# Kernel optimization log

Hardware: AMD Instinct MI355X
Metric: run time of the kernel (lower is better)

Reference implementation:

```python
import jax, jax.numpy as jnp
import numpy as np

# tiny-cuda-nn canonical 2D image hash-grid config
L = 16            # n_levels
F = 2             # n_features_per_level
T = 1 << 19       # hashmap size per level
BASE = 16         # base_resolution
SCALE = 1.5       # per_level_scale
HIDDEN = 64
ENC_DIM = L * F   # 32
OUT = 3           # rgb
S = 1024          # img_res / output_size
PRIME_Y = np.uint32(2654435761)


def setup_inputs() -> dict:
    key = jax.random.key(0)
    k1, k2, k3, k4 = jax.random.split(key, 4)
    # pixel-center grid exactly as in the torch module
    half = 0.5 / S
    xs = jnp.linspace(half, 1.0 - half, S, dtype=jnp.float32)
    xv, yv = jnp.meshgrid(xs, xs, indexing='ij')
    xy = jnp.stack([yv.flatten(), xv.flatten()], axis=1)  # [S*S, 2]
    # tcnn initializes hash tables ~ U(-1e-4, 1e-4)
    hash_tables = jax.random.uniform(k1, (L, T, F), jnp.float32, -1e-4, 1e-4)
    W0 = jax.random.normal(k2, (ENC_DIM, HIDDEN), jnp.float32) * np.sqrt(2.0 / ENC_DIM)
    W1 = jax.random.normal(k3, (HIDDEN, HIDDEN), jnp.float32) * np.sqrt(2.0 / HIDDEN)
    W2 = jax.random.normal(k4, (HIDDEN, OUT), jnp.float32) * np.sqrt(2.0 / HIDDEN)
    return {"xy": xy, "hash_tables": hash_tables, "W0": W0, "W1": W1, "W2": W2}


def _encode(xy, hash_tables):
    # multiresolution hash-grid encoding with bilinear interpolation
    resolutions = jnp.floor(BASE * SCALE ** jnp.arange(L)).astype(jnp.int32)  # [L]
    offs = jnp.array([[0, 0], [0, 1], [1, 0], [1, 1]], jnp.int32)            # [4,2]

    def level(table, res):
        pos = xy * res.astype(xy.dtype)            # [N,2]
        p0 = jnp.floor(pos).astype(jnp.int32)
        w = pos - p0                                # frac weights [N,2]
        corners = p0[:, None, :] + offs[None]       # [N,4,2]
        # hashed index (tcnn spatial hash): x*1 ^ y*PRIME, mod T
        cu = corners.astype(jnp.uint32)
        hidx = ((cu[..., 0] ^ (cu[..., 1] * PRIME_Y)) % np.uint32(T)).astype(jnp.int32)
        # dense index when the grid fits in the table
        didx = corners[..., 0] + corners[..., 1] * (res + 1)
        idx = jnp.where((res + 1) * (res + 1) <= T, didx, hidx)  # [N,4]
        f = table[idx]                               # [N,4,F] gather
        wx, wy = w[:, 0:1], w[:, 1:2]
        wts = jnp.stack([(1 - wx) * (1 - wy), (1 - wx) * wy,
                         wx * (1 - wy), wx * wy], axis=1)  # [N,4,1]
        return jnp.sum(f * wts, axis=1)              # [N,F]

    feats = jax.vmap(level, in_axes=(0, 0), out_axes=1)(hash_tables, resolutions)  # [N,L,F]
    return feats.reshape(feats.shape[0], ENC_DIM)


def reference(xy, hash_tables, W0, W1, W2):
    enc = _encode(xy, hash_tables)                  # [N,32]
    h = jax.nn.relu(enc @ W0)                       # tiny MLP, no bias (FullyFusedMLP)
    h = jax.nn.relu(h @ W1)
    out = h @ W2                                    # [N,3], linear output
    return out.reshape(S, S, OUT).transpose(2, 0, 1)  # [3,S,S]
```

## Files before the change

### kernel.cpp

```cpp
#include <hip/hip_runtime.h>
#include <cstdint>
#include <cstddef>

#define S_DIM 1024
#define NPTS (S_DIM * S_DIM)
#define NLEV 16
#define TBL (1u << 19)
#define TMASK (TBL - 1u)
#define PRIME_Y 2654435761u

typedef float v4f __attribute__((ext_vector_type(4)));
typedef short v8s __attribute__((ext_vector_type(8)));

__device__ __forceinline__ void split2(float a, float b, uint32_t& hi, uint32_t& lo) {
    uint32_t ua = __float_as_uint(a), ub = __float_as_uint(b);
    uint32_t ha = ua & 0xFFFF0000u, hb = ub & 0xFFFF0000u;
    float la = a - __uint_as_float(ha);
    float lb = b - __uint_as_float(hb);
    hi = (ha >> 16) | hb;
    lo = (__float_as_uint(la) >> 16) | (__float_as_uint(lb) & 0xFFFF0000u);
}

__global__ __launch_bounds__(256) void prep_weights(const float* __restrict__ W0,
                                                    const float* __restrict__ W1,
                                                    uint4* __restrict__ ws) {
    const int tid = threadIdx.x;
    const int lane = tid & 63;
    const int m = lane & 15, q = lane >> 4;

    {
        const int tile = tid >> 6;
        const int n = tile * 16 + m;
        uint32_t hi[4], lo[4];
        #pragma unroll
        for (int d = 0; d < 4; ++d) {
            const int k0 = q * 8 + 2 * d;
            split2(W0[k0 * 64 + n], W0[(k0 + 1) * 64 + n], hi[d], lo[d]);
        }
        ws[tid]       = make_uint4(hi[0], hi[1], hi[2], hi[3]);
        ws[256 + tid] = make_uint4(lo[0], lo[1], lo[2], lo[3]);
    }

    #pragma unroll
    for (int rep = 0; rep < 2; ++rep) {
        const int unit = tid + rep * 256;
        const int l2 = unit & 63, frag = unit >> 6;
        const int nt = frag >> 1, ks = frag & 1;
        const int mm = l2 & 15, qq = l2 >> 4;
        const int n = nt * 16 + mm;
        uint32_t hi[4], lo[4];
        #pragma unroll
        for (int d = 0; d < 4; ++d) {
            const int k0 = ks * 32 + qq * 8 + 2 * d;
            split2(W1[k0 * 64 + n], W1[(k0 + 1) * 64 + n], hi[d], lo[d]);
        }
        ws[512 + unit]  = make_uint4(hi[0], hi[1], hi[2], hi[3]);
        ws[1024 + unit] = make_uint4(lo[0], lo[1], lo[2], lo[3]);
    }
}

static __device__ __forceinline__ float2 level_feat(float x, float y, int res,
                                                    const float* __restrict__ tb) {
    const float fr = (float)res;
    const float px = x * fr, py = y * fr;
    const float fx = floorf(px), fy = floorf(py);
    const float wx = px - fx, wy = py - fy;
    const int x0 = (int)fx, y0 = (int)fy;

    int i00, i01, i10, i11;
    const bool dense = ((long long)(res + 1) * (long long)(res + 1) <= (long long)TBL);
    if (dense) {
        const int st = res + 1;
        i00 = x0 + y0 * st;
        i01 = i00 + st;
        i10 = i00 + 1;
        i11 = i01 + 1;
    } else {
        const unsigned a = (unsigned)x0, b = (unsigned)y0;
        const unsigned hb0 = b * PRIME_Y;
        const unsigned hb1 = (b + 1u) * PRIME_Y;
        i00 = (int)((a ^ hb0) & TMASK);
        i01 = (int)((a ^ hb1) & TMASK);
        i10 = (int)(((a + 1u) ^ hb0) & TMASK);
        i11 = (int)(((a + 1u) ^ hb1) & TMASK);
    }

    const float2 f00 = *(const float2*)(tb + 2 * (size_t)i00);
    const float2 f01 = *(const float2*)(tb + 2 * (size_t)i01);
    const float2 f10 = *(const float2*)(tb + 2 * (size_t)i10);
    const float2 f11 = *(const float2*)(tb + 2 * (size_t)i11);

    const float omx = 1.f - wx, omy = 1.f - wy;
    const float w00 = omx * omy, w01 = omx * wy, w10 = wx * omy, w11 = wx * wy;

    float2 e;
    e.x = f00.x * w00 + f01.x * w01 + f10.x * w10 + f11.x * w11;
    e.y = f00.y * w00 + f01.y * w01 + f10.y * w10 + f11.y * w11;
    return e;
}

__global__ __launch_bounds__(256, 2) void ngp_mfma(
    const float* __restrict__ xy,
    const float* __restrict__ tables,
    const float* __restrict__ W2,
    const uint4* __restrict__ ws,
    float* __restrict__ out)
{
    __shared__ alignas(16) uint32_t encLDS[256 * 36];
    __shared__ alignas(16) uint32_t h0LDS[4 * 16 * 68];
    __shared__ alignas(16) float w2t[3 * 64];

    const int tid = threadIdx.x;
    const int lane = tid & 63;
    const int wave = tid >> 6;
    const int m = lane & 15, q = lane >> 4;
    const int blockBase = blockIdx.x * 256;

    if (tid < 192) w2t[(tid % 3) * 64 + (tid / 3)] = W2[tid];

    {
        const int pid = blockBase + tid;
        const float2 p = ((const float2*)xy)[pid];
        constexpr int RES[NLEV] = {16, 24, 36, 54, 81, 121, 182, 273,
                                   410, 615, 922, 1383, 2075, 3113, 4670, 7006};
        float enc[32];
        #pragma unroll
        for (int l = 0; l < NLEV; ++l) {
            const float* tb = tables + (size_t)l * (size_t)(TBL * 2u);
            const float2 e = level_feat(p.x, p.y, RES[l], tb);
            enc[2 * l] = e.x;
            enc[2 * l + 1] = e.y;
        }
        uint32_t hi[16], lo[16];
        #pragma unroll
        for (int d = 0; d < 16; ++d) split2(enc[2 * d], enc[2 * d + 1], hi[d], lo[d]);
        uint32_t* row = encLDS + tid * 36;
        #pragma unroll
        for (int i = 0; i < 4; ++i) {
            *((uint4*)(row + 4 * i))      = make_uint4(hi[4*i], hi[4*i+1], hi[4*i+2], hi[4*i+3]);
            *((uint4*)(row + 16 + 4 * i)) = make_uint4(lo[4*i], lo[4*i+1], lo[4*i+2], lo[4*i+3]);
        }
    }

    __syncthreads();

    v8s w0h[4], w0l[4], w1h[8], w1l[8];
    #pragma unroll
    for (int t = 0; t < 4; ++t) {
        w0h[t] = __builtin_bit_cast(v8s, ws[t * 64 + lane]);
        w0l[t] = __builtin_bit_cast(v8s, ws[256 + t * 64 + lane]);
    }
    #pragma unroll
    for (int f = 0; f < 8; ++f) {
        w1h[f] = __builtin_bit_cast(v8s, ws[512 + f * 64 + lane]);
        w1l[f] = __builtin_bit_cast(v8s, ws[1024 + f * 64 + lane]);
    }

    #pragma unroll 1
    for (int t = 0; t < 4; ++t) {
        const uint32_t* erow = encLDS + (wave * 64 + t * 16 + m) * 36;
        const v8s eH = __builtin_bit_cast(v8s, *((const uint4*)(erow + q * 4)));
        const v8s eL = __builtin_bit_cast(v8s, *((const uint4*)(erow + 16 + q * 4)));

        v4f acc0[4];
        #pragma unroll
        for (int nt = 0; nt < 4; ++nt) {
            v4f c = {0.f, 0.f, 0.f, 0.f};
            c = __builtin_amdgcn_mfma_f32_16x16x32_bf16(w0l[nt], eH, c, 0, 0, 0);
            c = __builtin_amdgcn_mfma_f32_16x16x32_bf16(w0h[nt], eL, c, 0, 0, 0);
            c = __builtin_amdgcn_mfma_f32_16x16x32_bf16(w0h[nt], eH, c, 0, 0, 0);
            acc0[nt] = c;
        }

        uint32_t* hrow = h0LDS + (wave * 16 + m) * 68;
        #pragma unroll
        for (int nt = 0; nt < 4; ++nt) {
            const float r0 = fmaxf(acc0[nt][0], 0.f), r1 = fmaxf(acc0[nt][1], 0.f);
            const float r2 = fmaxf(acc0[nt][2], 0.f), r3 = fmaxf(acc0[nt][3], 0.f);
            uint32_t h0w, l0w, h1w, l1w;
            split2(r0, r1, h0w, l0w);
            split2(r2, r3, h1w, l1w);
            *((uint2*)(hrow + nt * 8 + q * 2))      = make_uint2(h0w, h1w);
            *((uint2*)(hrow + 32 + nt * 8 + q * 2)) = make_uint2(l0w, l1w);
        }

        const v8s b0H = __builtin_bit_cast(v8s, *((const uint4*)(hrow + q * 4)));
        const v8s b0L = __builtin_bit_cast(v8s, *((const uint4*)(hrow + 32 + q * 4)));
        const v8s b1H = __builtin_bit_cast(v8s, *((const uint4*)(hrow + 16 + q * 4)));
        const v8s b1L = __builtin_bit_cast(v8s, *((const uint4*)(hrow + 48 + q * 4)));

        v4f acc1[4];
        #pragma unroll
        for (int nt = 0; nt < 4; ++nt) {
            v4f c = {0.f, 0.f, 0.f, 0.f};
            c = __builtin_amdgcn_mfma_f32_16x16x32_bf16(w1l[nt*2+0], b0H, c, 0, 0, 0);
            c = __builtin_amdgcn_mfma_f32_16x16x32_bf16(w1h[nt*2+0], b0L, c, 0, 0, 0);
            c = __builtin_amdgcn_mfma_f32_16x16x32_bf16(w1h[nt*2+0], b0H, c, 0, 0, 0);
            c = __builtin_amdgcn_mfma_f32_16x16x32_bf16(w1l[nt*2+1], b1H, c, 0, 0, 0);
            c = __builtin_amdgcn_mfma_f32_16x16x32_bf16(w1h[nt*2+1], b1L, c, 0, 0, 0);
            c = __builtin_amdgcn_mfma_f32_16x16x32_bf16(w1h[nt*2+1], b1H, c, 0, 0, 0);
            acc1[nt] = c;
        }

        float o0 = 0.f, o1 = 0.f, o2 = 0.f;
        #pragma unroll
        for (int nt = 0; nt < 4; ++nt) {
            const int n = nt * 16 + q * 4;
            const float4 wa = *((const float4*)(w2t + 0 * 64 + n));
            const float4 wb = *((const float4*)(w2t + 1 * 64 + n));
            const float4 wc = *((const float4*)(w2t + 2 * 64 + n));
            const float h0r = fmaxf(acc1[nt][0], 0.f), h1r = fmaxf(acc1[nt][1], 0.f);
            const float h2r = fmaxf(acc1[nt][2], 0.f), h3r = fmaxf(acc1[nt][3], 0.f);
            o0 = fmaf(h0r, wa.x, fmaf(h1r, wa.y, fmaf(h2r, wa.z, fmaf(h3r, wa.w, o0))));
            o1 = fmaf(h0r, wb.x, fmaf(h1r, wb.y, fmaf(h2r, wb.z, fmaf(h3r, wb.w, o1))));
            o2 = fmaf(h0r, wc.x, fmaf(h1r, wc.y, fmaf(h2r, wc.z, fmaf(h3r, wc.w, o2))));
        }
        o0 += __shfl_xor(o0, 16); o0 += __shfl_xor(o0, 32);
        o1 += __shfl_xor(o1, 16); o1 += __shfl_xor(o1, 32);
        o2 += __shfl_xor(o2, 16); o2 += __shfl_xor(o2, 32);

        if (lane < 16) {
            const int p = blockBase + wave * 64 + t * 16 + lane;
            out[p] = o0;
            out[NPTS + p] = o1;
            out[2 * NPTS + p] = o2;
        }
    }
}

extern "C" void kernel_launch(void* const* d_in, const int* in_sizes, int n_in,
                              void* d_out, int out_size, void* d_ws, size_t ws_size,
                              hipStream_t stream) {
    const float* xy     = (const float*)d_in[0];
    const float* tables = (const float*)d_in[1];
    const float* W0     = (const float*)d_in[2];
    const float* W1     = (const float*)d_in[3];
    const float* W2     = (const float*)d_in[4];
    float* out = (float*)d_out;
    uint4* ws  = (uint4*)d_ws;

    hipLaunchKernelGGL(prep_weights, dim3(1), dim3(256), 0, stream, W0, W1, ws);
    hipLaunchKernelGGL(ngp_mfma, dim3(NPTS / 256), dim3(256), 0, stream,
                       xy, tables, W2, ws, out);
}
```

Before: 177.8 us.

## Encode directly into MFMA fragments, stage W1 in LDS, raise occupancy

Each lane now computes hash-grid features for 4 levels of its own MFMA row and packs them straight into the bf16 hi/lo B operands. This removes the encoding staging buffer in LDS and its barrier round-trip. W1 fragments move from registers to LDS and are reloaded per tile, and launch bounds rise to 4 blocks per CU, aiming for more waves in flight to hide the random gather latency. The trade-off is extra LDS reads in the second layer and a different gather pattern: each lane touches 4 levels for 4 points instead of 16 levels for one point.

```diff
diff --git a/kernel.cpp b/kernel.cpp
--- a/kernel.cpp
+++ b/kernel.cpp
@@ -99,16 +99,17 @@
     return e;
 }
 
-__global__ __launch_bounds__(256, 2) void ngp_mfma(
+__global__ __launch_bounds__(256, 4) void ngp_mfma(
     const float* __restrict__ xy,
     const float* __restrict__ tables,
     const float* __restrict__ W2,
     const uint4* __restrict__ ws,
     float* __restrict__ out)
 {
-    __shared__ alignas(16) uint32_t encLDS[256 * 36];
     __shared__ alignas(16) uint32_t h0LDS[4 * 16 * 68];
+    __shared__ alignas(16) uint4 w1LDS[1024];
     __shared__ alignas(16) float w2t[3 * 64];
+    __shared__ alignas(16) int resLDS[16];
 
     const int tid = threadIdx.x;
     const int lane = tid & 63;
@@ -117,58 +118,56 @@
     const int blockBase = blockIdx.x * 256;
 
     if (tid < 192) w2t[(tid % 3) * 64 + (tid / 3)] = W2[tid];
-
-    {
-        const int pid = blockBase + tid;
-        const float2 p = ((const float2*)xy)[pid];
+    if (tid < 16) {
         constexpr int RES[NLEV] = {16, 24, 36, 54, 81, 121, 182, 273,
                                    410, 615, 922, 1383, 2075, 3113, 4670, 7006};
-        float enc[32];
-        #pragma unroll
-        for (int l = 0; l < NLEV; ++l) {
-            const float* tb = tables + (size_t)l * (size_t)(TBL * 2u);
-            const float2 e = level_feat(p.x, p.y, RES[l], tb);
-            enc[2 * l] = e.x;
-            enc[2 * l + 1] = e.y;
-        }
-        uint32_t hi[16], lo[16];
-        #pragma unroll
-        for (int d = 0; d < 16; ++d) split2(enc[2 * d], enc[2 * d + 1], hi[d], lo[d]);
-        uint32_t* row = encLDS + tid * 36;
+        resLDS[tid] = RES[tid];
+    }
+    #pragma unroll
+    for (int i = 0; i < 4; ++i) w1LDS[tid + 256 * i] = ws[512 + tid + 256 * i];
+
+    v8s w0h[4], w0l[4];
+    #pragma unroll
+    for (int tt = 0; tt < 4; ++tt) {
+        w0h[tt] = __builtin_bit_cast(v8s, ws[tt * 64 + lane]);
+        w0l[tt] = __builtin_bit_cast(v8s, ws[256 + tt * 64 + lane]);
+    }
+
+    __syncthreads();
+
+    const int4 rq = *((const int4*)(resLDS + 4 * q));
+    const float* tb0 = tables + (size_t)(4 * q) * (size_t)(TBL * 2u);
+    const int rr[4] = {rq.x, rq.y, rq.z, rq.w};
+
+    v8s eH[4], eL[4];
+    #pragma unroll
+    for (int t = 0; t < 4; ++t) {
+        const int pid = blockBase + wave * 64 + t * 16 + m;
+        const float2 p = ((const float2*)xy)[pid];
+        float ef[8];
         #pragma unroll
         for (int i = 0; i < 4; ++i) {
-            *((uint4*)(row + 4 * i))      = make_uint4(hi[4*i], hi[4*i+1], hi[4*i+2], hi[4*i+3]);
-            *((uint4*)(row + 16 + 4 * i)) = make_uint4(lo[4*i], lo[4*i+1], lo[4*i+2], lo[4*i+3]);
-        }
-    }
-
-    __syncthreads();
-
-    v8s w0h[4], w0l[4], w1h[8], w1l[8];
+            const float2 e = level_feat(p.x, p.y, rr[i],
+                                        tb0 + (size_t)i * (size_t)(TBL * 2u));
+            ef[2 * i]     = e.x;
+            ef[2 * i + 1] = e.y;
+        }
+        uint32_t hi[4], lo[4];
+        #pragma unroll
+        for (int d = 0; d < 4; ++d) split2(ef[2 * d], ef[2 * d + 1], hi[d], lo[d]);
+        eH[t] = __builtin_bit_cast(v8s, make_uint4(hi[0], hi[1], hi[2], hi[3]));
+        eL[t] = __builtin_bit_cast(v8s, make_uint4(lo[0], lo[1], lo[2], lo[3]));
+    }
+
     #pragma unroll
     for (int t = 0; t < 4; ++t) {
-        w0h[t] = __builtin_bit_cast(v8s, ws[t * 64 + lane]);
-        w0l[t] = __builtin_bit_cast(v8s, ws[256 + t * 64 + lane]);
-    }
-    #pragma unroll
-    for (int f = 0; f < 8; ++f) {
-        w1h[f] = __builtin_bit_cast(v8s, ws[512 + f * 64 + lane]);
-        w1l[f] = __builtin_bit_cast(v8s, ws[1024 + f * 64 + lane]);
-    }
-
-    #pragma unroll 1
-    for (int t = 0; t < 4; ++t) {
-        const uint32_t* erow = encLDS + (wave * 64 + t * 16 + m) * 36;
-        const v8s eH = __builtin_bit_cast(v8s, *((const uint4*)(erow + q * 4)));
-        const v8s eL = __builtin_bit_cast(v8s, *((const uint4*)(erow + 16 + q * 4)));
-
         v4f acc0[4];
         #pragma unroll
         for (int nt = 0; nt < 4; ++nt) {
             v4f c = {0.f, 0.f, 0.f, 0.f};
-            c = __builtin_amdgcn_mfma_f32_16x16x32_bf16(w0l[nt], eH, c, 0, 0, 0);
-            c = __builtin_amdgcn_mfma_f32_16x16x32_bf16(w0h[nt], eL, c, 0, 0, 0);
-            c = __builtin_amdgcn_mfma_f32_16x16x32_bf16(w0h[nt], eH, c, 0, 0, 0);
+            c = __builtin_amdgcn_mfma_f32_16x16x32_bf16(w0l[nt], eH[t], c, 0, 0, 0);
+            c = __builtin_amdgcn_mfma_f32_16x16x32_bf16(w0h[nt], eL[t], c, 0, 0, 0);
+            c = __builtin_amdgcn_mfma_f32_16x16x32_bf16(w0h[nt], eH[t], c, 0, 0, 0);
             acc0[nt] = c;
         }
 
@@ -192,13 +191,17 @@
         v4f acc1[4];
         #pragma unroll
         for (int nt = 0; nt < 4; ++nt) {
+            const v8s a0h = __builtin_bit_cast(v8s, w1LDS[(nt * 2 + 0) * 64 + lane]);
+            const v8s a0l = __builtin_bit_cast(v8s, w1LDS[512 + (nt * 2 + 0) * 64 + lane]);
+            const v8s a1h = __builtin_bit_cast(v8s, w1LDS[(nt * 2 + 1) * 64 + lane]);
+            const v8s a1l = __builtin_bit_cast(v8s, w1LDS[512 + (nt * 2 + 1) * 64 + lane]);
             v4f c = {0.f, 0.f, 0.f, 0.f};
-            c = __builtin_amdgcn_mfma_f32_16x16x32_bf16(w1l[nt*2+0], b0H, c, 0, 0, 0);
-            c = __builtin_amdgcn_mfma_f32_16x16x32_bf16(w1h[nt*2+0], b0L, c, 0, 0, 0);
-            c = __builtin_amdgcn_mfma_f32_16x16x32_bf16(w1h[nt*2+0], b0H, c, 0, 0, 0);
-            c = __builtin_amdgcn_mfma_f32_16x16x32_bf16(w1l[nt*2+1], b1H, c, 0, 0, 0);
-            c = __builtin_amdgcn_mfma_f32_16x16x32_bf16(w1h[nt*2+1], b1L, c, 0, 0, 0);
-            c = __builtin_amdgcn_mfma_f32_16x16x32_bf16(w1h[nt*2+1], b1H, c, 0, 0, 0);
+            c = __builtin_amdgcn_mfma_f32_16x16x32_bf16(a0l, b0H, c, 0, 0, 0);
+            c = __builtin_amdgcn_mfma_f32_16x16x32_bf16(a0h, b0L, c, 0, 0, 0);
+            c = __builtin_amdgcn_mfma_f32_16x16x32_bf16(a0h, b0H, c, 0, 0, 0);
+            c = __builtin_amdgcn_mfma_f32_16x16x32_bf16(a1l, b1H, c, 0, 0, 0);
+            c = __builtin_amdgcn_mfma_f32_16x16x32_bf16(a1h, b1L, c, 0, 0, 0);
+            c = __builtin_amdgcn_mfma_f32_16x16x32_bf16(a1h, b1H, c, 0, 0, 0);
             acc1[nt] = c;
         }
 
```

Result: slower. 313.4 us (+76.2%).

## Stream W1/W2 weights from cache to free registers and raise occupancy

Applied to the files above, without the earlier changes.

The W1 MFMA fragments are no longer kept in registers for the whole kernel. They are reloaded from the workspace inside the tile loop, with an empty asm offset that stops the compiler from hoisting them back out. W2 is read straight from global memory, which removes the LDS staging buffer and the block-wide barrier. Launch bounds rise from 2 to 3 blocks per CU, aiming at more waves in flight to hide latency on the hash-table gathers. The cost is extra global/L1 load traffic and load latency inside the MLP loop.

```diff
diff --git a/kernel.cpp b/kernel.cpp
--- a/kernel.cpp
+++ b/kernel.cpp
@@ -99,7 +99,7 @@
     return e;
 }
 
-__global__ __launch_bounds__(256, 2) void ngp_mfma(
+__global__ __launch_bounds__(256, 3) void ngp_mfma(
     const float* __restrict__ xy,
     const float* __restrict__ tables,
     const float* __restrict__ W2,
@@ -108,15 +108,12 @@
 {
     __shared__ alignas(16) uint32_t encLDS[256 * 36];
     __shared__ alignas(16) uint32_t h0LDS[4 * 16 * 68];
-    __shared__ alignas(16) float w2t[3 * 64];
 
     const int tid = threadIdx.x;
     const int lane = tid & 63;
     const int wave = tid >> 6;
     const int m = lane & 15, q = lane >> 4;
     const int blockBase = blockIdx.x * 256;
-
-    if (tid < 192) w2t[(tid % 3) * 64 + (tid / 3)] = W2[tid];
 
     {
         const int pid = blockBase + tid;
@@ -142,22 +139,20 @@
         }
     }
 
-    __syncthreads();
-
-    v8s w0h[4], w0l[4], w1h[8], w1l[8];
+    v8s w0h[4], w0l[4];
     #pragma unroll
     for (int t = 0; t < 4; ++t) {
         w0h[t] = __builtin_bit_cast(v8s, ws[t * 64 + lane]);
         w0l[t] = __builtin_bit_cast(v8s, ws[256 + t * 64 + lane]);
     }
-    #pragma unroll
-    for (int f = 0; f < 8; ++f) {
-        w1h[f] = __builtin_bit_cast(v8s, ws[512 + f * 64 + lane]);
-        w1l[f] = __builtin_bit_cast(v8s, ws[1024 + f * 64 + lane]);
-    }
+
+    uint32_t* hrow = h0LDS + (wave * 16 + m) * 68;
 
     #pragma unroll 1
     for (int t = 0; t < 4; ++t) {
+        int tOff = 0;
+        asm volatile("" : "+v"(tOff));
+
         const uint32_t* erow = encLDS + (wave * 64 + t * 16 + m) * 36;
         const v8s eH = __builtin_bit_cast(v8s, *((const uint4*)(erow + q * 4)));
         const v8s eL = __builtin_bit_cast(v8s, *((const uint4*)(erow + 16 + q * 4)));
@@ -172,7 +167,6 @@
             acc0[nt] = c;
         }
 
-        uint32_t* hrow = h0LDS + (wave * 16 + m) * 68;
         #pragma unroll
         for (int nt = 0; nt < 4; ++nt) {
             const float r0 = fmaxf(acc0[nt][0], 0.f), r1 = fmaxf(acc0[nt][1], 0.f);
@@ -192,28 +186,32 @@
         v4f acc1[4];
         #pragma unroll
         for (int nt = 0; nt < 4; ++nt) {
+            const v8s a0h = __builtin_bit_cast(v8s, ws[512  + tOff + (nt * 2 + 0) * 64 + lane]);
+            const v8s a0l = __builtin_bit_cast(v8s, ws[1024 + tOff + (nt * 2 + 0) * 64 + lane]);
+            const v8s a1h = __builtin_bit_cast(v8s, ws[512  + tOff + (nt * 2 + 1) * 64 + lane]);
+            const v8s a1l = __builtin_bit_cast(v8s, ws[1024 + tOff + (nt * 2 + 1) * 64 + lane]);
             v4f c = {0.f, 0.f, 0.f, 0.f};
-            c = __builtin_amdgcn_mfma_f32_16x16x32_bf16(w1l[nt*2+0], b0H, c, 0, 0, 0);
-            c = __builtin_amdgcn_mfma_f32_16x16x32_bf16(w1h[nt*2+0], b0L, c, 0, 0, 0);
-            c = __builtin_amdgcn_mfma_f32_16x16x32_bf16(w1h[nt*2+0], b0H, c, 0, 0, 0);
-            c = __builtin_amdgcn_mfma_f32_16x16x32_bf16(w1l[nt*2+1], b1H, c, 0, 0, 0);
-            c = __builtin_amdgcn_mfma_f32_16x16x32_bf16(w1h[nt*2+1], b1L, c, 0, 0, 0);
-            c = __builtin_amdgcn_mfma_f32_16x16x32_bf16(w1h[nt*2+1], b1H, c, 0, 0, 0);
+            c = __builtin_amdgcn_mfma_f32_16x16x32_bf16(a0l, b0H, c, 0, 0, 0);
+            c = __builtin_amdgcn_mfma_f32_16x16x32_bf16(a0h, b0L, c, 0, 0, 0);
+            c = __builtin_amdgcn_mfma_f32_16x16x32_bf16(a0h, b0H, c, 0, 0, 0);
+            c = __builtin_amdgcn_mfma_f32_16x16x32_bf16(a1l, b1H, c, 0, 0, 0);
+            c = __builtin_amdgcn_mfma_f32_16x16x32_bf16(a1h, b1L, c, 0, 0, 0);
+            c = __builtin_amdgcn_mfma_f32_16x16x32_bf16(a1h, b1H, c, 0, 0, 0);
             acc1[nt] = c;
         }
 
         float o0 = 0.f, o1 = 0.f, o2 = 0.f;
         #pragma unroll
         for (int nt = 0; nt < 4; ++nt) {
-            const int n = nt * 16 + q * 4;
-            const float4 wa = *((const float4*)(w2t + 0 * 64 + n));
-            const float4 wb = *((const float4*)(w2t + 1 * 64 + n));
-            const float4 wc = *((const float4*)(w2t + 2 * 64 + n));
+            const int n0 = nt * 16 + q * 4;
+            const float4 g0 = *((const float4*)(W2 + n0 * 3 + tOff));
+            const float4 g1 = *((const float4*)(W2 + n0 * 3 + tOff + 4));
+            const float4 g2 = *((const float4*)(W2 + n0 * 3 + tOff + 8));
             const float h0r = fmaxf(acc1[nt][0], 0.f), h1r = fmaxf(acc1[nt][1], 0.f);
             const float h2r = fmaxf(acc1[nt][2], 0.f), h3r = fmaxf(acc1[nt][3], 0.f);
-            o0 = fmaf(h0r, wa.x, fmaf(h1r, wa.y, fmaf(h2r, wa.z, fmaf(h3r, wa.w, o0))));
-            o1 = fmaf(h0r, wb.x, fmaf(h1r, wb.y, fmaf(h2r, wb.z, fmaf(h3r, wb.w, o1))));
-            o2 = fmaf(h0r, wc.x, fmaf(h1r, wc.y, fmaf(h2r, wc.z, fmaf(h3r, wc.w, o2))));
+            o0 = fmaf(h0r, g0.x, fmaf(h1r, g0.w, fmaf(h2r, g1.z, fmaf(h3r, g2.y, o0))));
+            o1 = fmaf(h0r, g0.y, fmaf(h1r, g1.x, fmaf(h2r, g1.w, fmaf(h3r, g2.z, o1))));
+            o2 = fmaf(h0r, g0.z, fmaf(h1r, g1.y, fmaf(h2r, g2.x, fmaf(h3r, g2.w, o2))));
         }
         o0 += __shfl_xor(o0, 16); o0 += __shfl_xor(o0, 32);
         o1 += __shfl_xor(o1, 16); o1 += __shfl_xor(o1, 32);
```

New measurement: 200.9 us. +13.0%, slower.

## Split second-layer K into halves to shrink LDS staging and raise occupancy

Applied to the files above, without the earlier changes.

Layer 1 activations are now staged through LDS in two 32-wide K halves instead of one 64-wide buffer, halving the per-wave h0 scratch and accumulating acc1 across the two halves. Launch bounds move from 2 to 3 blocks per SIMD and a sched_barrier is placed after the encoding sync. The aim is more waves in flight to hide the latency of the random hash-table gathers. In exchange the register budget per thread is tighter, which risks spills given the many weight fragments held in registers, and there are more LDS round trips per tile.

```diff
diff --git a/kernel.cpp b/kernel.cpp
--- a/kernel.cpp
+++ b/kernel.cpp
@@ -99,7 +99,7 @@
     return e;
 }
 
-__global__ __launch_bounds__(256, 2) void ngp_mfma(
+__global__ __launch_bounds__(256, 3) void ngp_mfma(
     const float* __restrict__ xy,
     const float* __restrict__ tables,
     const float* __restrict__ W2,
@@ -107,7 +107,7 @@
     float* __restrict__ out)
 {
     __shared__ alignas(16) uint32_t encLDS[256 * 36];
-    __shared__ alignas(16) uint32_t h0LDS[4 * 16 * 68];
+    __shared__ alignas(16) uint32_t h0LDS[4 * 16 * 36];
     __shared__ alignas(16) float w2t[3 * 64];
 
     const int tid = threadIdx.x;
@@ -144,6 +144,8 @@
 
     __syncthreads();
 
+    __builtin_amdgcn_sched_barrier(0);
+
     v8s w0h[4], w0l[4], w1h[8], w1l[8];
     #pragma unroll
     for (int t = 0; t < 4; ++t) {
@@ -155,6 +157,8 @@
         w1h[f] = __builtin_bit_cast(v8s, ws[512 + f * 64 + lane]);
         w1l[f] = __builtin_bit_cast(v8s, ws[1024 + f * 64 + lane]);
     }
+
+    uint32_t* hrow = h0LDS + (wave * 16 + m) * 36;
 
     #pragma unroll 1
     for (int t = 0; t < 4; ++t) {
@@ -172,34 +176,34 @@
             acc0[nt] = c;
         }
 
-        uint32_t* hrow = h0LDS + (wave * 16 + m) * 68;
-        #pragma unroll
-        for (int nt = 0; nt < 4; ++nt) {
-            const float r0 = fmaxf(acc0[nt][0], 0.f), r1 = fmaxf(acc0[nt][1], 0.f);
-            const float r2 = fmaxf(acc0[nt][2], 0.f), r3 = fmaxf(acc0[nt][3], 0.f);
-            uint32_t h0w, l0w, h1w, l1w;
-            split2(r0, r1, h0w, l0w);
-            split2(r2, r3, h1w, l1w);
-            *((uint2*)(hrow + nt * 8 + q * 2))      = make_uint2(h0w, h1w);
-            *((uint2*)(hrow + 32 + nt * 8 + q * 2)) = make_uint2(l0w, l1w);
-        }
-
-        const v8s b0H = __builtin_bit_cast(v8s, *((const uint4*)(hrow + q * 4)));
-        const v8s b0L = __builtin_bit_cast(v8s, *((const uint4*)(hrow + 32 + q * 4)));
-        const v8s b1H = __builtin_bit_cast(v8s, *((const uint4*)(hrow + 16 + q * 4)));
-        const v8s b1L = __builtin_bit_cast(v8s, *((const uint4*)(hrow + 48 + q * 4)));
-
         v4f acc1[4];
         #pragma unroll
-        for (int nt = 0; nt < 4; ++nt) {
-            v4f c = {0.f, 0.f, 0.f, 0.f};
-            c = __builtin_amdgcn_mfma_f32_16x16x32_bf16(w1l[nt*2+0], b0H, c, 0, 0, 0);
-            c = __builtin_amdgcn_mfma_f32_16x16x32_bf16(w1h[nt*2+0], b0L, c, 0, 0, 0);
-            c = __builtin_amdgcn_mfma_f32_16x16x32_bf16(w1h[nt*2+0], b0H, c, 0, 0, 0);
-            c = __builtin_amdgcn_mfma_f32_16x16x32_bf16(w1l[nt*2+1], b1H, c, 0, 0, 0);
-            c = __builtin_amdgcn_mfma_f32_16x16x32_bf16(w1h[nt*2+1], b1L, c, 0, 0, 0);
-            c = __builtin_amdgcn_mfma_f32_16x16x32_bf16(w1h[nt*2+1], b1H, c, 0, 0, 0);
-            acc1[nt] = c;
+        for (int nt = 0; nt < 4; ++nt) acc1[nt] = (v4f){0.f, 0.f, 0.f, 0.f};
+
+        #pragma unroll
+        for (int ks = 0; ks < 2; ++ks) {
+            #pragma unroll
+            for (int nh = 0; nh < 2; ++nh) {
+                const int nt = ks * 2 + nh;
+                const float r0 = fmaxf(acc0[nt][0], 0.f), r1 = fmaxf(acc0[nt][1], 0.f);
+                const float r2 = fmaxf(acc0[nt][2], 0.f), r3 = fmaxf(acc0[nt][3], 0.f);
+                uint32_t h0w, l0w, h1w, l1w;
+                split2(r0, r1, h0w, l0w);
+                split2(r2, r3, h1w, l1w);
+                *((uint2*)(hrow + nh * 8 + q * 2))      = make_uint2(h0w, h1w);
+                *((uint2*)(hrow + 16 + nh * 8 + q * 2)) = make_uint2(l0w, l1w);
+            }
+            const v8s bH = __builtin_bit_cast(v8s, *((const uint4*)(hrow + q * 4)));
+            const v8s bL = __builtin_bit_cast(v8s, *((const uint4*)(hrow + 16 + q * 4)));
+
+            #pragma unroll
+            for (int nt = 0; nt < 4; ++nt) {
+                v4f c = acc1[nt];
+                c = __builtin_amdgcn_mfma_f32_16x16x32_bf16(w1l[nt*2+ks], bH, c, 0, 0, 0);
+                c = __builtin_amdgcn_mfma_f32_16x16x32_bf16(w1h[nt*2+ks], bL, c, 0, 0, 0);
+                c = __builtin_amdgcn_mfma_f32_16x16x32_bf16(w1h[nt*2+ks], bH, c, 0, 0, 0);
+                acc1[nt] = c;
+            }
         }
 
         float o0 = 0.f, o1 = 0.f, o2 = 0.f;
```

After: 202.3 us. 1.14x slower.
